# Kernel optimization log

Measured on AMD Instinct MI355X. Metric: run time of the kernel, lower is better.

## Reference

```python
import jax, jax.numpy as jnp
import numpy as np

N = 100_000      # nodes
E = 1_600_000    # edges (no self loops; reference appends them)
G = 1_000        # graphs
FIN = 27         # input node features
HID = 128        # hidden_channels
L = 4            # num_layers
H = 8            # num_heads
B = 4            # num_bases
A = 3            # aggregators: sum, mean, max
FH = HID // H    # per-head out dim
EPS = 1e-5


def setup_inputs() -> dict:
    key = jax.random.key(0)
    ks = jax.random.split(key, 16)
    s = 0.05
    x = jax.random.normal(ks[0], (N, FIN), jnp.float32)
    src = jax.random.randint(ks[1], (E,), 0, N)
    off = jax.random.randint(ks[2], (E,), 1, N)
    dst = (src + off) % N  # guaranteed no self loops
    edge_index = jnp.stack([src, dst]).astype(jnp.int64)
    batch = jnp.sort(jax.random.randint(ks[3], (N,), 0, G)).astype(jnp.int64)
    return {
        "x": x,
        "lin1_w": jax.random.normal(ks[4], (FIN, HID), jnp.float32) * s,
        "lin1_b": jnp.zeros((HID,), jnp.float32),
        "bn1_g": jnp.ones((HID,), jnp.float32),
        "bn1_b": jnp.zeros((HID,), jnp.float32),
        "bases_w": jax.random.normal(ks[5], (L, HID, B * FH), jnp.float32) * s,
        "comb_w": jax.random.normal(ks[6], (L, HID, H * B * A), jnp.float32) * s,
        "comb_b": jnp.zeros((L, H * B * A), jnp.float32),
        "conv_bias": jnp.zeros((L, HID), jnp.float32),
        "bn_g": jnp.ones((L, HID), jnp.float32),
        "bn_b": jnp.zeros((L, HID), jnp.float32),
        "mlp_w1": jax.random.normal(ks[7], (HID, HID // 2), jnp.float32) * s,
        "mbn1_g": jnp.ones((HID // 2,), jnp.float32),
        "mbn1_b": jnp.zeros((HID // 2,), jnp.float32),
        "mlp_w2": jax.random.normal(ks[8], (HID // 2, HID // 4), jnp.float32) * s,
        "mbn2_g": jnp.ones((HID // 4,), jnp.float32),
        "mbn2_b": jnp.zeros((HID // 4,), jnp.float32),
        "mlp_w3": jax.random.normal(ks[9], (HID // 4, 10), jnp.float32) * s,
        "mlp_b3": jnp.zeros((10,), jnp.float32),
        "edge_index": edge_index,
        "batch": batch,
    }


def _bn(h, g, b):
    # BatchNorm1d, training mode (biased batch variance), per-feature over nodes
    mu = jnp.mean(h, axis=0)
    var = jnp.mean((h - mu) ** 2, axis=0)
    return g * (h - mu) * jax.lax.rsqrt(var + EPS) + b


def reference(x, lin1_w, lin1_b, bn1_g, bn1_b, bases_w, comb_w, comb_b,
              conv_bias, bn_g, bn_b, mlp_w1, mbn1_g, mbn1_b, mlp_w2,
              mbn2_g, mbn2_b, mlp_w3, mlp_b3, edge_index, batch):
    # add self loops (inputs contain none, matching remove+add in EGConv)
    loop = jnp.arange(N, dtype=edge_index.dtype)
    src = jnp.concatenate([edge_index[0], loop])
    dst = jnp.concatenate([edge_index[1], loop])

    h = jax.nn.relu(_bn(x @ lin1_w + lin1_b, bn1_g, bn1_b))  # [N, HID]

    ones_e = jnp.ones((src.shape[0], 1), h.dtype)
    deg = jax.ops.segment_sum(ones_e, dst, num_segments=N)  # [N,1], >=1 via self loops

    for l in range(L):
        bases = h @ bases_w[l]                              # [N, B*FH]
        comb = (h @ comb_w[l] + comb_b[l]).reshape(N, H, A * B)
        msg = bases[src]                                    # [E+N, B*FH]
        ssum = jax.ops.segment_sum(msg, dst, num_segments=N)
        smean = ssum / deg
        smax = jax.ops.segment_max(msg, dst, num_segments=N)
        agg = jnp.stack([ssum, smean, smax], axis=1)        # [N, A, B*FH]
        agg = agg.reshape(N, A * B, FH)
        out = jnp.einsum('nhk,nkf->nhf', comb, agg).reshape(N, HID) + conv_bias[l]
        h = h + jax.nn.relu(_bn(out, bn_g[l], bn_b[l]))

    # global mean pool over graphs
    gsum = jax.ops.segment_sum(h, batch, num_segments=G)
    gcnt = jnp.maximum(jax.ops.segment_sum(jnp.ones((N, 1), h.dtype), batch, num_segments=G), 1.0)
    g = gsum / gcnt                                         # [G, HID]

    g = jax.nn.relu(_bn(g @ mlp_w1, mbn1_g, mbn1_b))
    g = jax.nn.relu(_bn(g @ mlp_w2, mbn2_g, mbn2_b))
    return g @ mlp_w3 + mlp_b3                              # [G, 10]
```

## Files before the change

### kernel.cpp

```cpp
#include <hip/hip_runtime.h>

#define EPSV 1e-5f
#define NEGINF -3.402823466e38f
#define NBMAX 1600
#define CHUNK 8192
#define CAP3 6144

typedef short bf16x8 __attribute__((ext_vector_type(8)));
typedef float f32x4 __attribute__((ext_vector_type(4)));

__device__ __forceinline__ unsigned short f2bf(float f) {
    union { float f; unsigned i; } c; c.f = f;
    unsigned r = c.i + 0x7fff + ((c.i >> 16) & 1);
    return (unsigned short)(r >> 16);
}
__device__ __forceinline__ float blo(unsigned u) {
    union { unsigned i; float f; } c; c.i = u << 16; return c.f;
}
__device__ __forceinline__ float bhi(unsigned u) {
    union { unsigned i; float f; } c; c.i = u & 0xffff0000u; return c.f;
}

__global__ __launch_bounds__(256)
void k_lin1(const float* __restrict__ x, const float* __restrict__ w,
            const float* __restrict__ bvec, float* __restrict__ outb,
            float* __restrict__ stats, int N)
{
    __shared__ float wl[27 * 128];
    int tid = threadIdx.x;
    for (int i = tid; i < 27 * 128; i += 256) wl[i] = w[i];
    __syncthreads();

    int l  = tid & 63;
    int wv = tid >> 6;
    float bv0 = bvec[l], bv1 = bvec[64 + l];
    int waveSlots = gridDim.x * 4;
    int trips = (N + waveSlots - 1) / waveSlots;
    float s0 = 0.f, q0 = 0.f, s1 = 0.f, q1 = 0.f;
    for (int it = 0; it < trips; ++it) {
        int n = (it * gridDim.x + blockIdx.x) * 4 + wv;
        if (n < N) {
            const float* xr = x + (size_t)n * 27;
            float a0 = bv0, a1 = bv1;
            #pragma unroll
            for (int k = 0; k < 27; ++k) {
                float xv = xr[k];
                a0 = fmaf(xv, wl[k * 128 + l], a0);
                a1 = fmaf(xv, wl[k * 128 + 64 + l], a1);
            }
            outb[(size_t)n * 128 + l] = a0;
            outb[(size_t)n * 128 + 64 + l] = a1;
            s0 += a0; q0 += a0 * a0; s1 += a1; q1 += a1 * a1;
        }
    }
    __shared__ float sred[4][256];
    sred[0][tid] = s0; sred[1][tid] = q0;
    sred[2][tid] = s1; sred[3][tid] = q1;
    __syncthreads();
    if (tid < 64) {
        int t = tid;
        float v0 = sred[0][t] + sred[0][t + 64] + sred[0][t + 128] + sred[0][t + 192];
        float v1 = sred[1][t] + sred[1][t + 64] + sred[1][t + 128] + sred[1][t + 192];
        float v2 = sred[2][t] + sred[2][t + 64] + sred[2][t + 128] + sred[2][t + 192];
        float v3 = sred[3][t] + sred[3][t + 64] + sred[3][t + 128] + sred[3][t + 192];
        atomicAdd(stats + t, v0);
        atomicAdd(stats + 128 + t, v1);
        atomicAdd(stats + 64 + t, v2);
        atomicAdd(stats + 192 + t, v3);
    }
}

__global__ __launch_bounds__(256)
void k_p1_hist(const int* __restrict__ dst, int* __restrict__ bcnt,
               int E, int NB, int shift)
{
    __shared__ int hist[NBMAX];
    for (int i = threadIdx.x; i < NB; i += 256) hist[i] = 0;
    __syncthreads();
    int stride = gridDim.x * 256;
    for (int e = blockIdx.x * 256 + threadIdx.x; e < E; e += stride)
        atomicAdd(&hist[dst[e] >> shift], 1);
    __syncthreads();
    for (int i = threadIdx.x; i < NB; i += 256)
        if (hist[i]) atomicAdd(bcnt + i, hist[i]);
}

__global__ void k_scan1(const int* __restrict__ cnt, int* __restrict__ rowptr,
                        int* __restrict__ bsum, int N)
{
    __shared__ int sb[256];
    int i = blockIdx.x * 256 + threadIdx.x;
    int v = (i < N) ? cnt[i] : 0;
    sb[threadIdx.x] = v;
    __syncthreads();
    for (int ofs = 1; ofs < 256; ofs <<= 1) {
        int u = (threadIdx.x >= ofs) ? sb[threadIdx.x - ofs] : 0;
        __syncthreads();
        sb[threadIdx.x] += u;
        __syncthreads();
    }
    if (i < N) rowptr[i] = sb[threadIdx.x] - v;
    if (threadIdx.x == 255) bsum[blockIdx.x] = sb[255];
}

__global__ void k_scan2(int* __restrict__ bs, int nb)
{
    __shared__ int sb[512];
    int t = threadIdx.x;
    int v = (t < nb) ? bs[t] : 0;
    sb[t] = v;
    __syncthreads();
    for (int ofs = 1; ofs < 512; ofs <<= 1) {
        int u = (t >= ofs) ? sb[t - ofs] : 0;
        __syncthreads();
        sb[t] += u;
        __syncthreads();
    }
    bs[t] = sb[t] - v;
}

__global__ void k_scan3(int* __restrict__ rowptr, const int* __restrict__ bsum,
                        int N, int E)
{
    int i = blockIdx.x * blockDim.x + threadIdx.x;
    if (i < N) rowptr[i] += bsum[i >> 8];
    if (i == 0) rowptr[N] = E;
}

__global__ __launch_bounds__(256)
void k_p2_scatter(const int* __restrict__ src, const int* __restrict__ dst,
                  const int* __restrict__ bbase, int* __restrict__ bcur0,
                  uint2* __restrict__ bucketed, int E, int NB, int shift)
{
    __shared__ uint2 ebuf[CHUNK];
    __shared__ int hist[NBMAX];
    __shared__ int cur[NBMAX];
    __shared__ int wtmp[256];
    int tid = threadIdx.x;
    int c0 = blockIdx.x * CHUNK;
    int cc = min(CHUNK, E - c0);
    if (cc <= 0) return;

    for (int i = tid; i < NB; i += 256) hist[i] = 0;
    __syncthreads();
    for (int i = tid; i < cc; i += 256)
        atomicAdd(&hist[dst[c0 + i] >> shift], 1);
    __syncthreads();
    int per = (NB + 255) / 256;
    int beg = tid * per, end = min(beg + per, NB);
    int s = 0;
    for (int i = beg; i < end; ++i) s += hist[i];
    wtmp[tid] = s;
    __syncthreads();
    for (int ofs = 1; ofs < 256; ofs <<= 1) {
        int u = (tid >= ofs) ? wtmp[tid - ofs] : 0;
        __syncthreads();
        wtmp[tid] += u;
        __syncthreads();
    }
    int run = wtmp[tid] - s;
    for (int i = beg; i < end; ++i) { cur[i] = run; run += hist[i]; }
    __syncthreads();
    for (int i = tid; i < cc; i += 256) {
        int sv = src[c0 + i], dv = dst[c0 + i];
        int b = dv >> shift;
        int pos = atomicAdd(&cur[b], 1);
        ebuf[pos] = make_uint2((unsigned)sv, (unsigned)dv);
    }
    __syncthreads();
    for (int b = tid; b < NB; b += 256) {
        int c = hist[b];
        if (c > 0) {
            int lb = cur[b] - c;
            int gb = bbase[b] + atomicAdd(&bcur0[b], c);
            hist[b] = gb - lb;
        }
    }
    __syncthreads();
    for (int i = tid; i < cc; i += 256) {
        uint2 u = ebuf[i];
        int b = (int)(u.y >> shift);
        bucketed[hist[b] + i] = u;
    }
}

__global__ __launch_bounds__(256)
void k_p3_csr(const uint2* __restrict__ bucketed, const int* __restrict__ bbase,
              int* __restrict__ rowptr, int* __restrict__ csr,
              int N, int NB, int shift)
{
    __shared__ int ncnt[128], nsc[128];
    __shared__ int lcsr[CAP3];
    int b = blockIdx.x;
    int tid = threadIdx.x;
    int e0 = bbase[b], e1 = bbase[b + 1];
    int cnt = e1 - e0;
    int node0 = b << shift;
    int nodes = min(1 << shift, N - node0);

    if (tid < 128) ncnt[tid] = 0;
    __syncthreads();
    for (int i = tid; i < cnt; i += 256)
        atomicAdd(&ncnt[(int)bucketed[e0 + i].y - node0], 1);
    __syncthreads();
    if (tid < 128) nsc[tid] = ncnt[tid];
    __syncthreads();
    for (int ofs = 1; ofs < 128; ofs <<= 1) {
        int u = 0;
        if (tid < 128 && tid >= ofs) u = nsc[tid - ofs];
        __syncthreads();
        if (tid < 128) nsc[tid] += u;
        __syncthreads();
    }
    if (tid < nodes) rowptr[node0 + tid] = e0 + nsc[tid] - ncnt[tid];
    if (tid == 0 && b == NB - 1) rowptr[N] = e1;
    if (tid < 128) ncnt[tid] = nsc[tid] - ncnt[tid];
    __syncthreads();
    if (cnt <= CAP3) {
        for (int i = tid; i < cnt; i += 256) {
            uint2 u = bucketed[e0 + i];
            int d = (int)u.y - node0;
            int pos = atomicAdd(&ncnt[d], 1);
            lcsr[pos] = (int)u.x;
        }
        __syncthreads();
        for (int i = tid; i < cnt; i += 256) csr[e0 + i] = lcsr[i];
    } else {
        for (int i = tid; i < cnt; i += 256) {
            uint2 u = bucketed[e0 + i];
            int d = (int)u.y - node0;
            int pos = atomicAdd(&ncnt[d], 1);
            csr[e0 + pos] = (int)u.x;
        }
    }
}

__global__ __launch_bounds__(256)
void k_gemm_mfma(const float* __restrict__ tin, float* __restrict__ h,
                 const float* __restrict__ stats, const float* __restrict__ gamma,
                 const float* __restrict__ beta, float invN, int residual,
                 const float* __restrict__ basesW, const float* __restrict__ combW,
                 const float* __restrict__ combB,
                 unsigned short* __restrict__ basesP,
                 unsigned short* __restrict__ combB16, int N)
{
    __shared__ unsigned short Wlds[2560 * 8];
    __shared__ float scL[128], shL[128];
    int tid = threadIdx.x;
    if (tid < 128) {
        float mu  = stats[tid] * invN;
        float var = stats[128 + tid] * invN - mu * mu;
        float sc  = gamma[tid] * rsqrtf(var + EPSV);
        scL[tid] = sc;
        shL[tid] = beta[tid] - mu * sc;
    }
    for (int i = tid; i < 2560; i += 256) {
        int ct = i >> 8, rem = i & 255;
        int ln = rem & 63;
        int n16 = ln & 15, quad = ln >> 4;
        int k = ((rem >> 6) << 5) + quad * 8;
        unsigned short tmp[8];
        if (ct < 4) {
            int c = ct * 16 + n16;
            #pragma unroll
            for (int j = 0; j < 8; ++j) tmp[j] = f2bf(basesW[(k + j) * 64 + c]);
        } else {
            int c = (ct - 4) * 16 + n16;
            #pragma unroll
            for (int j = 0; j < 8; ++j) tmp[j] = f2bf(combW[(k + j) * 96 + c]);
        }
        uint4 pk;
        pk.x = (unsigned)tmp[0] | ((unsigned)tmp[1] << 16);
        pk.y = (unsigned)tmp[2] | ((unsigned)tmp[3] << 16);
        pk.z = (unsigned)tmp[4] | ((unsigned)tmp[5] << 16);
        pk.w = (unsigned)tmp[6] | ((unsigned)tmp[7] << 16);
        *(uint4*)&Wlds[(size_t)i * 8] = pk;
    }
    __syncthreads();

    int lane = tid & 63, wv = tid >> 6;
    int f = lane & 15, quad = lane >> 4;
    float cbv[6];
    #pragma unroll
    for (int s = 0; s < 6; ++s) cbv[s] = combB[s * 16 + f];

    int tiles = (N + 15) >> 4;
    int waveSlots = gridDim.x * 4;
    for (int tile = blockIdx.x * 4 + wv; tile < tiles; tile += waveSlots) {
        int tb = tile * 16;
        int mnode = min(tb + f, N - 1);
        size_t rbase = (size_t)mnode * 128;

        f32x4 acc[10];
        #pragma unroll
        for (int ct = 0; ct < 10; ++ct) acc[ct] = (f32x4){0.f, 0.f, 0.f, 0.f};

        #pragma unroll
        for (int ki = 0; ki < 4; ++ki) {
            int kc = quad * 8 + ki * 32;
            float4 t0 = *(const float4*)&tin[rbase + kc];
            float4 t1 = *(const float4*)&tin[rbase + kc + 4];
            float4 r0, r1;
            r0.x = fmaxf(t0.x * scL[kc]     + shL[kc],     0.f);
            r0.y = fmaxf(t0.y * scL[kc + 1] + shL[kc + 1], 0.f);
            r0.z = fmaxf(t0.z * scL[kc + 2] + shL[kc + 2], 0.f);
            r0.w = fmaxf(t0.w * scL[kc + 3] + shL[kc + 3], 0.f);
            r1.x = fmaxf(t1.x * scL[kc + 4] + shL[kc + 4], 0.f);
            r1.y = fmaxf(t1.y * scL[kc + 5] + shL[kc + 5], 0.f);
            r1.z = fmaxf(t1.z * scL[kc + 6] + shL[kc + 6], 0.f);
            r1.w = fmaxf(t1.w * scL[kc + 7] + shL[kc + 7], 0.f);
            if (residual) {
                float4 h0 = *(const float4*)&h[rbase + kc];
                float4 h1 = *(const float4*)&h[rbase + kc + 4];
                r0.x += h0.x; r0.y += h0.y; r0.z += h0.z; r0.w += h0.w;
                r1.x += h1.x; r1.y += h1.y; r1.z += h1.z; r1.w += h1.w;
            }
            *(float4*)&h[rbase + kc] = r0;
            *(float4*)&h[rbase + kc + 4] = r1;
            short ab[8];
            ab[0] = (short)f2bf(r0.x); ab[1] = (short)f2bf(r0.y);
            ab[2] = (short)f2bf(r0.z); ab[3] = (short)f2bf(r0.w);
            ab[4] = (short)f2bf(r1.x); ab[5] = (short)f2bf(r1.y);
            ab[6] = (short)f2bf(r1.z); ab[7] = (short)f2bf(r1.w);
            bf16x8 a = *(bf16x8*)ab;
            #pragma unroll
            for (int ct = 0; ct < 10; ++ct) {
                bf16x8 bfr = *(const bf16x8*)&Wlds[(size_t)((ct * 4 + ki) * 64 + lane) * 8];
                acc[ct] = __builtin_amdgcn_mfma_f32_16x16x32_bf16(a, bfr, acc[ct], 0, 0, 0);
            }
        }

        #pragma unroll
        for (int r = 0; r < 4; ++r) {
            int node = tb + quad * 4 + r;
            if (node < N) {
                #pragma unroll
                for (int ct = 0; ct < 4; ++ct)
                    basesP[(size_t)node * 64 + f * 4 + ct] = f2bf(acc[ct][r]);
                #pragma unroll
                for (int s = 0; s < 6; ++s)
                    combB16[(size_t)node * 96 + s * 16 + f] = f2bf(acc[4 + s][r] + cbv[s]);
            }
        }
    }
}

__global__ __launch_bounds__(256)
void k_agg(const unsigned short* __restrict__ basesP, const unsigned short* __restrict__ combB16,
           const int* __restrict__ csr, const int* __restrict__ rowptr,
           const float* __restrict__ cbias, float* __restrict__ outb,
           float* __restrict__ stats, int N)
{
    int l = threadIdx.x & 63;
    int w = threadIdx.x >> 6;
    int f = l & 15, sub = l >> 4;
    const char* bp = (const char*)basesP;
    unsigned fof = (unsigned)(f << 3);
    float cb0 = cbias[l], cb1 = cbias[64 + l];
    int waveSlots = gridDim.x * 4;
    int trips = (N + waveSlots - 1) / waveSlots;
    float s0 = 0.f, q0 = 0.f, s1 = 0.f, q1 = 0.f;

    for (int it = 0; it < trips; ++it) {
        int n = (it * gridDim.x + blockIdx.x) * 4 + w;
        if (n < N) {
            int row0 = rowptr[n], row1 = rowptr[n + 1];
            int cnt = row1 - row0;
            float S0 = 0.f, S1 = 0.f, S2 = 0.f, S3 = 0.f;
            float M0 = NEGINF, M1 = NEGINF, M2 = NEGINF, M3 = NEGINF;
            const int* cs = csr + row0 + sub;
            int tfull = cnt >> 2;
            #pragma unroll 4
            for (int t = 0; t < tfull; ++t) {
                int sn = cs[4 * t];
                uint2 u = *(const uint2*)(bp + (((unsigned)sn) << 7) + fof);
                float v0 = blo(u.x), v1 = bhi(u.x), v2 = blo(u.y), v3 = bhi(u.y);
                S0 += v0; S1 += v1; S2 += v2; S3 += v3;
                M0 = fmaxf(M0, v0); M1 = fmaxf(M1, v1);
                M2 = fmaxf(M2, v2); M3 = fmaxf(M3, v3);
            }
            int rem = cnt & 3;
            if (rem) {
                int e = (cnt & ~3) + sub;
                int sn = csr[row0 + min(e, cnt - 1)];
                uint2 u = *(const uint2*)(bp + (((unsigned)sn) << 7) + fof);
                if (sub < rem) {
                    float v0 = blo(u.x), v1 = bhi(u.x), v2 = blo(u.y), v3 = bhi(u.y);
                    S0 += v0; S1 += v1; S2 += v2; S3 += v3;
                    M0 = fmaxf(M0, v0); M1 = fmaxf(M1, v1);
                    M2 = fmaxf(M2, v2); M3 = fmaxf(M3, v3);
                }
            }
            S0 += __shfl_xor(S0, 16, 64); S1 += __shfl_xor(S1, 16, 64);
            S2 += __shfl_xor(S2, 16, 64); S3 += __shfl_xor(S3, 16, 64);
            S0 += __shfl_xor(S0, 32, 64); S1 += __shfl_xor(S1, 32, 64);
            S2 += __shfl_xor(S2, 32, 64); S3 += __shfl_xor(S3, 32, 64);
            M0 = fmaxf(M0, __shfl_xor(M0, 16, 64)); M1 = fmaxf(M1, __shfl_xor(M1, 16, 64));
            M2 = fmaxf(M2, __shfl_xor(M2, 16, 64)); M3 = fmaxf(M3, __shfl_xor(M3, 16, 64));
            M0 = fmaxf(M0, __shfl_xor(M0, 32, 64)); M1 = fmaxf(M1, __shfl_xor(M1, 32, 64));
            M2 = fmaxf(M2, __shfl_xor(M2, 32, 64)); M3 = fmaxf(M3, __shfl_xor(M3, 32, 64));
            uint2 su = *(const uint2*)(bp + (((unsigned)n) << 7) + fof);
            float w0 = blo(su.x), w1 = bhi(su.x), w2 = blo(su.y), w3 = bhi(su.y);
            S0 += w0; S1 += w1; S2 += w2; S3 += w3;
            M0 = fmaxf(M0, w0); M1 = fmaxf(M1, w1);
            M2 = fmaxf(M2, w2); M3 = fmaxf(M3, w3);
            float invd = 1.f / (float)(cnt + 1);
            float A0 = S0 * invd, A1 = S1 * invd, A2 = S2 * invd, A3 = S3 * invd;

            const unsigned short* cr = combB16 + (size_t)n * 96;
            const uint2* c0p = (const uint2*)(cr + sub * 12);
            const uint2* c1p = (const uint2*)(cr + 48 + sub * 12);
            uint2 qa0 = c0p[0], qa1 = c0p[1], qa2 = c0p[2];
            uint2 qb0 = c1p[0], qb1 = c1p[1], qb2 = c1p[2];

            float o0 = cb0, o1 = cb1;
            o0 = fmaf(blo(qa0.x), S0, o0); o0 = fmaf(bhi(qa0.x), S1, o0);
            o0 = fmaf(blo(qa0.y), S2, o0); o0 = fmaf(bhi(qa0.y), S3, o0);
            o0 = fmaf(blo(qa1.x), A0, o0); o0 = fmaf(bhi(qa1.x), A1, o0);
            o0 = fmaf(blo(qa1.y), A2, o0); o0 = fmaf(bhi(qa1.y), A3, o0);
            o0 = fmaf(blo(qa2.x), M0, o0); o0 = fmaf(bhi(qa2.x), M1, o0);
            o0 = fmaf(blo(qa2.y), M2, o0); o0 = fmaf(bhi(qa2.y), M3, o0);
            o1 = fmaf(blo(qb0.x), S0, o1); o1 = fmaf(bhi(qb0.x), S1, o1);
            o1 = fmaf(blo(qb0.y), S2, o1); o1 = fmaf(bhi(qb0.y), S3, o1);
            o1 = fmaf(blo(qb1.x), A0, o1); o1 = fmaf(bhi(qb1.x), A1, o1);
            o1 = fmaf(blo(qb1.y), A2, o1); o1 = fmaf(bhi(qb1.y), A3, o1);
            o1 = fmaf(blo(qb2.x), M0, o1); o1 = fmaf(bhi(qb2.x), M1, o1);
            o1 = fmaf(blo(qb2.y), M2, o1); o1 = fmaf(bhi(qb2.y), M3, o1);

            outb[(size_t)n * 128 + l] = o0;
            outb[(size_t)n * 128 + 64 + l] = o1;
            s0 += o0; q0 += o0 * o0; s1 += o1; q1 += o1 * o1;
        }
    }
    __shared__ float sred[4][256];
    sred[0][threadIdx.x] = s0; sred[1][threadIdx.x] = q0;
    sred[2][threadIdx.x] = s1; sred[3][threadIdx.x] = q1;
    __syncthreads();
    if (threadIdx.x < 64) {
        int t = threadIdx.x;
        float v0 = sred[0][t] + sred[0][t + 64] + sred[0][t + 128] + sred[0][t + 192];
        float v1 = sred[1][t] + sred[1][t + 64] + sred[1][t + 128] + sred[1][t + 192];
        float v2 = sred[2][t] + sred[2][t + 64] + sred[2][t + 128] + sred[2][t + 192];
        float v3 = sred[3][t] + sred[3][t + 64] + sred[3][t + 128] + sred[3][t + 192];
        atomicAdd(stats + t, v0);
        atomicAdd(stats + 128 + t, v1);
        atomicAdd(stats + 64 + t, v2);
        atomicAdd(stats + 192 + t, v3);
    }
}

__global__ void k_gbound(const int* __restrict__ batch, int* __restrict__ gstart,
                         int N, int G)
{
    int stride = gridDim.x * blockDim.x;
    for (int n = blockIdx.x * blockDim.x + threadIdx.x; n < N; n += stride) {
        int b = batch[n];
        if (n == 0) {
            for (int g = 0; g <= b; ++g) gstart[g] = 0;
        } else {
            int pb = batch[n - 1];
            for (int g = pb + 1; g <= b; ++g) gstart[g] = n;
        }
        if (n == N - 1) {
            for (int g = b + 1; g <= G; ++g) gstart[g] = N;
        }
    }
}

__global__ __launch_bounds__(256)
void k_gmean(const float* __restrict__ t, const float* __restrict__ h,
             const float* __restrict__ stats, const float* __restrict__ gamma,
             const float* __restrict__ beta, float invN,
             const int* __restrict__ gstart, float* __restrict__ gout, int G)
{
    __shared__ float part[128];
    int g = blockIdx.x;
    if (g >= G) return;
    int c = threadIdx.x & 127;
    int half = threadIdx.x >> 7;
    float mu  = stats[c] * invN;
    float var = stats[128 + c] * invN - mu * mu;
    float sc  = gamma[c] * rsqrtf(var + EPSV);
    float sh  = beta[c] - mu * sc;
    int s = gstart[g], e = gstart[g + 1];
    float acc = 0.f;
    #pragma unroll 2
    for (int n = s + half; n < e; n += 2) {
        size_t o = (size_t)n * 128 + c;
        acc += h[o] + fmaxf(t[o] * sc + sh, 0.f);
    }
    if (half) part[c] = acc;
    __syncthreads();
    if (!half) {
        float tot = acc + part[c];
        float cntf = fmaxf((float)(e - s), 1.f);
        gout[g * 128 + c] = tot / cntf;
    }
}

__global__ void k_mlp1(const float* __restrict__ gin, const float* __restrict__ w1,
                       float* __restrict__ t1, float* __restrict__ stats, int G)
{
    int g = blockIdx.x;
    int c = threadIdx.x;
    const float* gr = gin + g * 128;
    float acc = 0.f;
    for (int k = 0; k < 128; ++k) acc = fmaf(gr[k], w1[k * 64 + c], acc);
    t1[g * 64 + c] = acc;
    atomicAdd(stats + c, acc);
    atomicAdd(stats + 64 + c, acc * acc);
}

__global__ void k_mlp2(const float* __restrict__ t1, const float* __restrict__ stats1,
                       const float* __restrict__ g1, const float* __restrict__ b1,
                       const float* __restrict__ w2, float* __restrict__ t2,
                       float* __restrict__ stats2, float invG, int G)
{
    __shared__ float row[64];
    int g = blockIdx.x;
    int c = threadIdx.x;
    float v = t1[g * 64 + c];
    float mu = stats1[c] * invG;
    float var = stats1[64 + c] * invG - mu * mu;
    row[c] = fmaxf(g1[c] * (v - mu) * rsqrtf(var + EPSV) + b1[c], 0.f);
    __syncthreads();
    if (c < 32) {
        float acc = 0.f;
        #pragma unroll
        for (int k = 0; k < 64; ++k) acc = fmaf(row[k], w2[k * 32 + c], acc);
        t2[g * 32 + c] = acc;
        atomicAdd(stats2 + c, acc);
        atomicAdd(stats2 + 32 + c, acc * acc);
    }
}

__global__ void k_mlp3(const float* __restrict__ t2, const float* __restrict__ stats2,
                       const float* __restrict__ g2, const float* __restrict__ b2,
                       const float* __restrict__ w3, const float* __restrict__ b3,
                       float* __restrict__ out, float invG, int G)
{
    __shared__ float row[32];
    int g = blockIdx.x;
    int c = threadIdx.x;
    if (c < 32) {
        float v = t2[g * 32 + c];
        float mu = stats2[c] * invG;
        float var = stats2[32 + c] * invG - mu * mu;
        row[c] = fmaxf(g2[c] * (v - mu) * rsqrtf(var + EPSV) + b2[c], 0.f);
    }
    __syncthreads();
    if (c < 10) {
        float acc = b3[c];
        #pragma unroll
        for (int k = 0; k < 32; ++k) acc = fmaf(row[k], w3[k * 10 + c], acc);
        out[g * 10 + c] = acc;
    }
}

extern "C" void kernel_launch(void* const* d_in, const int* in_sizes, int n_in,
                              void* d_out, int out_size, void* d_ws, size_t ws_size,
                              hipStream_t stream)
{
    const float* x        = (const float*)d_in[0];
    const float* lin1_w   = (const float*)d_in[1];
    const float* lin1_b   = (const float*)d_in[2];
    const float* bn1_g    = (const float*)d_in[3];
    const float* bn1_b    = (const float*)d_in[4];
    const float* bases_w  = (const float*)d_in[5];
    const float* comb_w   = (const float*)d_in[6];
    const float* comb_b   = (const float*)d_in[7];
    const float* conv_bias= (const float*)d_in[8];
    const float* bn_g     = (const float*)d_in[9];
    const float* bn_b     = (const float*)d_in[10];
    const float* mlp_w1   = (const float*)d_in[11];
    const float* mbn1_g   = (const float*)d_in[12];
    const float* mbn1_b   = (const float*)d_in[13];
    const float* mlp_w2   = (const float*)d_in[14];
    const float* mbn2_g   = (const float*)d_in[15];
    const float* mbn2_b   = (const float*)d_in[16];
    const float* mlp_w3   = (const float*)d_in[17];
    const float* mlp_b3   = (const float*)d_in[18];
    const int*   edge_idx = (const int*)d_in[19];
    const int*   batch    = (const int*)d_in[20];
    float* outp = (float*)d_out;

    const int N = in_sizes[20];
    const int E = in_sizes[19] / 2;
    const int G = out_size / 10;
    const int* esrc = edge_idx;
    const int* edst = edge_idx + E;

    int shift = 6;
    while ((((N - 1) >> shift) + 1) > NBMAX && shift < 7) ++shift;
    const int NB = ((N - 1) >> shift) + 1;

    char* p = (char*)d_ws;
    auto alloc = [&](size_t bytes) {
        char* r = p;
        p += (bytes + 255) & ~(size_t)255;
        return r;
    };
    float*          h      = (float*)alloc((size_t)N * 128 * 4);
    unsigned short* basesP = (unsigned short*)alloc((size_t)N * 64 * 2);
    unsigned short* combB16= (unsigned short*)alloc((size_t)N * 96 * 2);
    float*          outb   = (float*)alloc((size_t)N * 128 * 4);
    int*            csr    = (int*)  alloc((size_t)E * 4);
    int*            rowptr = (int*)  alloc((size_t)(N + 1) * 4);
    int*            bbase  = (int*)  alloc((size_t)(NB + 1) * 4);
    float*          tg     = (float*)alloc((size_t)G * 128 * 4);
    float*          t1     = (float*)alloc((size_t)G * 64 * 4);
    float*          t2     = (float*)alloc((size_t)G * 32 * 4);
    int*            gstart = (int*)  alloc((size_t)(G + 1) * 4);
    int*            bsum   = (int*)  alloc(512 * 4);
    char*           zbase  = p;
    int*            bcnt   = (int*)  alloc((size_t)NB * 4);
    int*            bcur0  = (int*)  alloc((size_t)NB * 4);
    float*          stats  = (float*)alloc(7 * 256 * 4);
    size_t zbytes = (size_t)(p - zbase);
    uint2* bucketed = (uint2*)combB16;
    (void)ws_size; (void)n_in;

    hipMemsetAsync(zbase, 0, zbytes, stream);

    const float invN = 1.0f / (float)N;
    const float invG = 1.0f / (float)G;
    const int nbB = (NB + 255) / 256;

    k_lin1<<<1024, 256, 0, stream>>>(x, lin1_w, lin1_b, outb, stats, N);
    k_p1_hist<<<256, 256, 0, stream>>>(edst, bcnt, E, NB, shift);
    k_scan1<<<nbB, 256, 0, stream>>>(bcnt, bbase, bsum, NB);
    k_scan2<<<1, 512, 0, stream>>>(bsum, nbB);
    k_scan3<<<nbB, 256, 0, stream>>>(bbase, bsum, NB, E);
    k_p2_scatter<<<(E + CHUNK - 1) / CHUNK, 256, 0, stream>>>(esrc, edst, bbase, bcur0,
                                                              bucketed, E, NB, shift);
    k_p3_csr<<<NB, 256, 0, stream>>>(bucketed, bbase, rowptr, csr, N, NB, shift);

    for (int l = 0; l < 4; ++l) {
        const float* bw = bases_w + (size_t)l * 128 * 64;
        const float* cw = comb_w + (size_t)l * 128 * 96;
        const float* cb = comb_b + (size_t)l * 96;
        const float* cvb = conv_bias + (size_t)l * 128;
        const float* pg = (l == 0) ? bn1_g : bn_g + (l - 1) * 128;
        const float* pb = (l == 0) ? bn1_b : bn_b + (l - 1) * 128;
        k_gemm_mfma<<<512, 256, 0, stream>>>(outb, h, stats + l * 256, pg, pb, invN,
                                             l > 0 ? 1 : 0, bw, cw, cb, basesP, combB16, N);
        k_agg<<<2048, 256, 0, stream>>>(basesP, combB16, csr, rowptr, cvb,
                                        outb, stats + (1 + l) * 256, N);
    }

    k_gbound<<<512, 256, 0, stream>>>(batch, gstart, N, G);
    k_gmean<<<G, 256, 0, stream>>>(outb, h, stats + 4 * 256, bn_g + 3 * 128,
                                   bn_b + 3 * 128, invN, gstart, tg, G);
    float* st5 = stats + 5 * 256;
    float* st6 = stats + 6 * 256;
    k_mlp1<<<G, 64, 0, stream>>>(tg, mlp_w1, t1, st5, G);
    k_mlp2<<<G, 64, 0, stream>>>(t1, st5, mbn1_g, mbn1_b, mlp_w2, t2, st6, invG, G);
    k_mlp3<<<G, 64, 0, stream>>>(t2, st6, mbn2_g, mbn2_b, mlp_w3, mlp_b3, outp, invG, G);
}
```

Before: 818.1 us.

## Store pre-BN conv output in bf16 and batch four nodes per wave in aggregation

The intermediate pre-BatchNorm buffer (outb) is now stored as bf16 instead of fp32, which halves its write and read traffic in lin1, agg, gemm and gmean. The aggregation kernel now gives each wave four consecutive nodes and interleaves their neighbor gathers, so more independent loads are in flight per wave. It launches one block per 16 nodes instead of using a grid-stride loop. In exchange, the BN input loses precision, and nodes with uneven degrees waste lanes because each wave loops to the largest count among its four nodes.

```diff
diff --git a/kernel.cpp b/kernel.cpp
--- a/kernel.cpp
+++ b/kernel.cpp
@@ -20,10 +20,13 @@
 __device__ __forceinline__ float bhi(unsigned u) {
     union { unsigned i; float f; } c; c.i = u & 0xffff0000u; return c.f;
 }
+__device__ __forceinline__ float bfu(unsigned short u) {
+    union { unsigned i; float f; } c; c.i = ((unsigned)u) << 16; return c.f;
+}
 
 __global__ __launch_bounds__(256)
 void k_lin1(const float* __restrict__ x, const float* __restrict__ w,
-            const float* __restrict__ bvec, float* __restrict__ outb,
+            const float* __restrict__ bvec, unsigned short* __restrict__ outb,
             float* __restrict__ stats, int N)
 {
     __shared__ float wl[27 * 128];
@@ -48,8 +51,8 @@
                 a0 = fmaf(xv, wl[k * 128 + l], a0);
                 a1 = fmaf(xv, wl[k * 128 + 64 + l], a1);
             }
-            outb[(size_t)n * 128 + l] = a0;
-            outb[(size_t)n * 128 + 64 + l] = a1;
+            outb[(size_t)n * 128 + l] = f2bf(a0);
+            outb[(size_t)n * 128 + 64 + l] = f2bf(a1);
             s0 += a0; q0 += a0 * a0; s1 += a1; q1 += a1 * a1;
         }
     }
@@ -236,7 +239,7 @@
 }
 
 __global__ __launch_bounds__(256)
-void k_gemm_mfma(const float* __restrict__ tin, float* __restrict__ h,
+void k_gemm_mfma(const unsigned short* __restrict__ tin, float* __restrict__ h,
                  const float* __restrict__ stats, const float* __restrict__ gamma,
                  const float* __restrict__ beta, float invN, int residual,
                  const float* __restrict__ basesW, const float* __restrict__ combW,
@@ -298,30 +301,29 @@
         #pragma unroll
         for (int ki = 0; ki < 4; ++ki) {
             int kc = quad * 8 + ki * 32;
-            float4 t0 = *(const float4*)&tin[rbase + kc];
-            float4 t1 = *(const float4*)&tin[rbase + kc + 4];
-            float4 r0, r1;
-            r0.x = fmaxf(t0.x * scL[kc]     + shL[kc],     0.f);
-            r0.y = fmaxf(t0.y * scL[kc + 1] + shL[kc + 1], 0.f);
-            r0.z = fmaxf(t0.z * scL[kc + 2] + shL[kc + 2], 0.f);
-            r0.w = fmaxf(t0.w * scL[kc + 3] + shL[kc + 3], 0.f);
-            r1.x = fmaxf(t1.x * scL[kc + 4] + shL[kc + 4], 0.f);
-            r1.y = fmaxf(t1.y * scL[kc + 5] + shL[kc + 5], 0.f);
-            r1.z = fmaxf(t1.z * scL[kc + 6] + shL[kc + 6], 0.f);
-            r1.w = fmaxf(t1.w * scL[kc + 7] + shL[kc + 7], 0.f);
+            uint4 tv = *(const uint4*)&tin[rbase + kc];
+            float r0, r1, r2, r3, r4, r5, r6, r7;
+            r0 = fmaxf(blo(tv.x) * scL[kc]     + shL[kc],     0.f);
+            r1 = fmaxf(bhi(tv.x) * scL[kc + 1] + shL[kc + 1], 0.f);
+            r2 = fmaxf(blo(tv.y) * scL[kc + 2] + shL[kc + 2], 0.f);
+            r3 = fmaxf(bhi(tv.y) * scL[kc + 3] + shL[kc + 3], 0.f);
+            r4 = fmaxf(blo(tv.z) * scL[kc + 4] + shL[kc + 4], 0.f);
+            r5 = fmaxf(bhi(tv.z) * scL[kc + 5] + shL[kc + 5], 0.f);
+            r6 = fmaxf(blo(tv.w) * scL[kc + 6] + shL[kc + 6], 0.f);
+            r7 = fmaxf(bhi(tv.w) * scL[kc + 7] + shL[kc + 7], 0.f);
             if (residual) {
                 float4 h0 = *(const float4*)&h[rbase + kc];
                 float4 h1 = *(const float4*)&h[rbase + kc + 4];
-                r0.x += h0.x; r0.y += h0.y; r0.z += h0.z; r0.w += h0.w;
-                r1.x += h1.x; r1.y += h1.y; r1.z += h1.z; r1.w += h1.w;
+                r0 += h0.x; r1 += h0.y; r2 += h0.z; r3 += h0.w;
+                r4 += h1.x; r5 += h1.y; r6 += h1.z; r7 += h1.w;
             }
-            *(float4*)&h[rbase + kc] = r0;
-            *(float4*)&h[rbase + kc + 4] = r1;
+            *(float4*)&h[rbase + kc]     = make_float4(r0, r1, r2, r3);
+            *(float4*)&h[rbase + kc + 4] = make_float4(r4, r5, r6, r7);
             short ab[8];
-            ab[0] = (short)f2bf(r0.x); ab[1] = (short)f2bf(r0.y);
-            ab[2] = (short)f2bf(r0.z); ab[3] = (short)f2bf(r0.w);
-            ab[4] = (short)f2bf(r1.x); ab[5] = (short)f2bf(r1.y);
-            ab[6] = (short)f2bf(r1.z); ab[7] = (short)f2bf(r1.w);
+            ab[0] = (short)f2bf(r0); ab[1] = (short)f2bf(r1);
+            ab[2] = (short)f2bf(r2); ab[3] = (short)f2bf(r3);
+            ab[4] = (short)f2bf(r4); ab[5] = (short)f2bf(r5);
+            ab[6] = (short)f2bf(r6); ab[7] = (short)f2bf(r7);
             bf16x8 a = *(bf16x8*)ab;
             #pragma unroll
             for (int ct = 0; ct < 10; ++ct) {
@@ -348,7 +350,7 @@
 __global__ __launch_bounds__(256)
 void k_agg(const unsigned short* __restrict__ basesP, const unsigned short* __restrict__ combB16,
            const int* __restrict__ csr, const int* __restrict__ rowptr,
-           const float* __restrict__ cbias, float* __restrict__ outb,
+           const float* __restrict__ cbias, unsigned short* __restrict__ outb,
            float* __restrict__ stats, int N)
 {
     int l = threadIdx.x & 63;
@@ -356,80 +358,103 @@
     int f = l & 15, sub = l >> 4;
     const char* bp = (const char*)basesP;
     unsigned fof = (unsigned)(f << 3);
-    float cb0 = cbias[l], cb1 = cbias[64 + l];
-    int waveSlots = gridDim.x * 4;
-    int trips = (N + waveSlots - 1) / waveSlots;
     float s0 = 0.f, q0 = 0.f, s1 = 0.f, q1 = 0.f;
 
-    for (int it = 0; it < trips; ++it) {
-        int n = (it * gridDim.x + blockIdx.x) * 4 + w;
-        if (n < N) {
-            int row0 = rowptr[n], row1 = rowptr[n + 1];
-            int cnt = row1 - row0;
-            float S0 = 0.f, S1 = 0.f, S2 = 0.f, S3 = 0.f;
-            float M0 = NEGINF, M1 = NEGINF, M2 = NEGINF, M3 = NEGINF;
-            const int* cs = csr + row0 + sub;
-            int tfull = cnt >> 2;
-            #pragma unroll 4
-            for (int t = 0; t < tfull; ++t) {
-                int sn = cs[4 * t];
-                uint2 u = *(const uint2*)(bp + (((unsigned)sn) << 7) + fof);
-                float v0 = blo(u.x), v1 = bhi(u.x), v2 = blo(u.y), v3 = bhi(u.y);
-                S0 += v0; S1 += v1; S2 += v2; S3 += v3;
-                M0 = fmaxf(M0, v0); M1 = fmaxf(M1, v1);
-                M2 = fmaxf(M2, v2); M3 = fmaxf(M3, v3);
+    int base = (blockIdx.x * 4 + w) * 4;
+    if (base < N) {
+        float cb0 = cbias[l], cb1 = cbias[64 + l];
+        int row0[4], cnt[4];
+        #pragma unroll
+        for (int m = 0; m < 4; ++m) {
+            int nm = min(base + m, N - 1);
+            row0[m] = rowptr[nm];
+            cnt[m]  = rowptr[nm + 1] - row0[m];
+            if (base + m >= N) cnt[m] = 0;
+        }
+        float S[4][4], M[4][4];
+        #pragma unroll
+        for (int m = 0; m < 4; ++m) {
+            #pragma unroll
+            for (int v = 0; v < 4; ++v) { S[m][v] = 0.f; M[m][v] = NEGINF; }
+        }
+        int mc = max(max(cnt[0], cnt[1]), max(cnt[2], cnt[3]));
+        int mt = (mc + 3) >> 2;
+        int e = sub;
+        #pragma unroll 2
+        for (int t = 0; t < mt; ++t) {
+            int sn[4];
+            #pragma unroll
+            for (int m = 0; m < 4; ++m) {
+                int ce = min(e, cnt[m] - 1);
+                ce = max(ce, 0);
+                sn[m] = csr[row0[m] + ce];
             }
-            int rem = cnt & 3;
-            if (rem) {
-                int e = (cnt & ~3) + sub;
-                int sn = csr[row0 + min(e, cnt - 1)];
-                uint2 u = *(const uint2*)(bp + (((unsigned)sn) << 7) + fof);
-                if (sub < rem) {
-                    float v0 = blo(u.x), v1 = bhi(u.x), v2 = blo(u.y), v3 = bhi(u.y);
-                    S0 += v0; S1 += v1; S2 += v2; S3 += v3;
-                    M0 = fmaxf(M0, v0); M1 = fmaxf(M1, v1);
-                    M2 = fmaxf(M2, v2); M3 = fmaxf(M3, v3);
-                }
+            uint2 u[4];
+            #pragma unroll
+            for (int m = 0; m < 4; ++m)
+                u[m] = *(const uint2*)(bp + (((unsigned)sn[m]) << 7) + fof);
+            #pragma unroll
+            for (int m = 0; m < 4; ++m) {
+                bool val = e < cnt[m];
+                float v0 = blo(u[m].x), v1 = bhi(u[m].x);
+                float v2 = blo(u[m].y), v3 = bhi(u[m].y);
+                S[m][0] += val ? v0 : 0.f;
+                S[m][1] += val ? v1 : 0.f;
+                S[m][2] += val ? v2 : 0.f;
+                S[m][3] += val ? v3 : 0.f;
+                M[m][0] = fmaxf(M[m][0], val ? v0 : NEGINF);
+                M[m][1] = fmaxf(M[m][1], val ? v1 : NEGINF);
+                M[m][2] = fmaxf(M[m][2], val ? v2 : NEGINF);
+                M[m][3] = fmaxf(M[m][3], val ? v3 : NEGINF);
             }
-            S0 += __shfl_xor(S0, 16, 64); S1 += __shfl_xor(S1, 16, 64);
-            S2 += __shfl_xor(S2, 16, 64); S3 += __shfl_xor(S3, 16, 64);
-            S0 += __shfl_xor(S0, 32, 64); S1 += __shfl_xor(S1, 32, 64);
-            S2 += __shfl_xor(S2, 32, 64); S3 += __shfl_xor(S3, 32, 64);
-            M0 = fmaxf(M0, __shfl_xor(M0, 16, 64)); M1 = fmaxf(M1, __shfl_xor(M1, 16, 64));
-            M2 = fmaxf(M2, __shfl_xor(M2, 16, 64)); M3 = fmaxf(M3, __shfl_xor(M3, 16, 64));
-            M0 = fmaxf(M0, __shfl_xor(M0, 32, 64)); M1 = fmaxf(M1, __shfl_xor(M1, 32, 64));
-            M2 = fmaxf(M2, __shfl_xor(M2, 32, 64)); M3 = fmaxf(M3, __shfl_xor(M3, 32, 64));
-            uint2 su = *(const uint2*)(bp + (((unsigned)n) << 7) + fof);
-            float w0 = blo(su.x), w1 = bhi(su.x), w2 = blo(su.y), w3 = bhi(su.y);
-            S0 += w0; S1 += w1; S2 += w2; S3 += w3;
-            M0 = fmaxf(M0, w0); M1 = fmaxf(M1, w1);
-            M2 = fmaxf(M2, w2); M3 = fmaxf(M3, w3);
-            float invd = 1.f / (float)(cnt + 1);
-            float A0 = S0 * invd, A1 = S1 * invd, A2 = S2 * invd, A3 = S3 * invd;
-
-            const unsigned short* cr = combB16 + (size_t)n * 96;
-            const uint2* c0p = (const uint2*)(cr + sub * 12);
-            const uint2* c1p = (const uint2*)(cr + 48 + sub * 12);
-            uint2 qa0 = c0p[0], qa1 = c0p[1], qa2 = c0p[2];
-            uint2 qb0 = c1p[0], qb1 = c1p[1], qb2 = c1p[2];
-
-            float o0 = cb0, o1 = cb1;
-            o0 = fmaf(blo(qa0.x), S0, o0); o0 = fmaf(bhi(qa0.x), S1, o0);
-            o0 = fmaf(blo(qa0.y), S2, o0); o0 = fmaf(bhi(qa0.y), S3, o0);
-            o0 = fmaf(blo(qa1.x), A0, o0); o0 = fmaf(bhi(qa1.x), A1, o0);
-            o0 = fmaf(blo(qa1.y), A2, o0); o0 = fmaf(bhi(qa1.y), A3, o0);
-            o0 = fmaf(blo(qa2.x), M0, o0); o0 = fmaf(bhi(qa2.x), M1, o0);
-            o0 = fmaf(blo(qa2.y), M2, o0); o0 = fmaf(bhi(qa2.y), M3, o0);
-            o1 = fmaf(blo(qb0.x), S0, o1); o1 = fmaf(bhi(qb0.x), S1, o1);
-            o1 = fmaf(blo(qb0.y), S2, o1); o1 = fmaf(bhi(qb0.y), S3, o1);
-            o1 = fmaf(blo(qb1.x), A0, o1); o1 = fmaf(bhi(qb1.x), A1, o1);
-            o1 = fmaf(blo(qb1.y), A2, o1); o1 = fmaf(bhi(qb1.y), A3, o1);
-            o1 = fmaf(blo(qb2.x), M0, o1); o1 = fmaf(bhi(qb2.x), M1, o1);
-            o1 = fmaf(blo(qb2.y), M2, o1); o1 = fmaf(bhi(qb2.y), M3, o1);
-
-            outb[(size_t)n * 128 + l] = o0;
-            outb[(size_t)n * 128 + 64 + l] = o1;
-            s0 += o0; q0 += o0 * o0; s1 += o1; q1 += o1 * o1;
+            e += 4;
+        }
+        #pragma unroll
+        for (int m = 0; m < 4; ++m) {
+            int n = base + m;
+            if (n < N) {
+                float T0 = S[m][0], T1 = S[m][1], T2 = S[m][2], T3 = S[m][3];
+                float X0 = M[m][0], X1 = M[m][1], X2 = M[m][2], X3 = M[m][3];
+                T0 += __shfl_xor(T0, 16, 64); T1 += __shfl_xor(T1, 16, 64);
+                T2 += __shfl_xor(T2, 16, 64); T3 += __shfl_xor(T3, 16, 64);
+                T0 += __shfl_xor(T0, 32, 64); T1 += __shfl_xor(T1, 32, 64);
+                T2 += __shfl_xor(T2, 32, 64); T3 += __shfl_xor(T3, 32, 64);
+                X0 = fmaxf(X0, __shfl_xor(X0, 16, 64)); X1 = fmaxf(X1, __shfl_xor(X1, 16, 64));
+                X2 = fmaxf(X2, __shfl_xor(X2, 16, 64)); X3 = fmaxf(X3, __shfl_xor(X3, 16, 64));
+                X0 = fmaxf(X0, __shfl_xor(X0, 32, 64)); X1 = fmaxf(X1, __shfl_xor(X1, 32, 64));
+                X2 = fmaxf(X2, __shfl_xor(X2, 32, 64)); X3 = fmaxf(X3, __shfl_xor(X3, 32, 64));
+                uint2 su = *(const uint2*)(bp + (((unsigned)n) << 7) + fof);
+                float w0 = blo(su.x), w1 = bhi(su.x), w2 = blo(su.y), w3 = bhi(su.y);
+                T0 += w0; T1 += w1; T2 += w2; T3 += w3;
+                X0 = fmaxf(X0, w0); X1 = fmaxf(X1, w1);
+                X2 = fmaxf(X2, w2); X3 = fmaxf(X3, w3);
+                float invd = 1.f / (float)(cnt[m] + 1);
+                float A0 = T0 * invd, A1 = T1 * invd, A2 = T2 * invd, A3 = T3 * invd;
+
+                const unsigned short* cr = combB16 + (size_t)n * 96;
+                const uint2* c0p = (const uint2*)(cr + sub * 12);
+                const uint2* c1p = (const uint2*)(cr + 48 + sub * 12);
+                uint2 qa0 = c0p[0], qa1 = c0p[1], qa2 = c0p[2];
+                uint2 qb0 = c1p[0], qb1 = c1p[1], qb2 = c1p[2];
+
+                float o0 = cb0, o1 = cb1;
+                o0 = fmaf(blo(qa0.x), T0, o0); o0 = fmaf(bhi(qa0.x), T1, o0);
+                o0 = fmaf(blo(qa0.y), T2, o0); o0 = fmaf(bhi(qa0.y), T3, o0);
+                o0 = fmaf(blo(qa1.x), A0, o0); o0 = fmaf(bhi(qa1.x), A1, o0);
+                o0 = fmaf(blo(qa1.y), A2, o0); o0 = fmaf(bhi(qa1.y), A3, o0);
+                o0 = fmaf(blo(qa2.x), X0, o0); o0 = fmaf(bhi(qa2.x), X1, o0);
+                o0 = fmaf(blo(qa2.y), X2, o0); o0 = fmaf(bhi(qa2.y), X3, o0);
+                o1 = fmaf(blo(qb0.x), T0, o1); o1 = fmaf(bhi(qb0.x), T1, o1);
+                o1 = fmaf(blo(qb0.y), T2, o1); o1 = fmaf(bhi(qb0.y), T3, o1);
+                o1 = fmaf(blo(qb1.x), A0, o1); o1 = fmaf(bhi(qb1.x), A1, o1);
+                o1 = fmaf(blo(qb1.y), A2, o1); o1 = fmaf(bhi(qb1.y), A3, o1);
+                o1 = fmaf(blo(qb2.x), X0, o1); o1 = fmaf(bhi(qb2.x), X1, o1);
+                o1 = fmaf(blo(qb2.y), X2, o1); o1 = fmaf(bhi(qb2.y), X3, o1);
+
+                outb[(size_t)n * 128 + l] = f2bf(o0);
+                outb[(size_t)n * 128 + 64 + l] = f2bf(o1);
+                s0 += o0; q0 += o0 * o0; s1 += o1; q1 += o1 * o1;
+            }
         }
     }
     __shared__ float sred[4][256];
@@ -468,7 +493,7 @@
 }
 
 __global__ __launch_bounds__(256)
-void k_gmean(const float* __restrict__ t, const float* __restrict__ h,
+void k_gmean(const unsigned short* __restrict__ t, const float* __restrict__ h,
              const float* __restrict__ stats, const float* __restrict__ gamma,
              const float* __restrict__ beta, float invN,
              const int* __restrict__ gstart, float* __restrict__ gout, int G)
@@ -487,7 +512,7 @@
     #pragma unroll 2
     for (int n = s + half; n < e; n += 2) {
         size_t o = (size_t)n * 128 + c;
-        acc += h[o] + fmaxf(t[o] * sc + sh, 0.f);
+        acc += h[o] + fmaxf(bfu(t[o]) * sc + sh, 0.f);
     }
     if (half) part[c] = acc;
     __syncthreads();
@@ -603,8 +628,8 @@
     float*          h      = (float*)alloc((size_t)N * 128 * 4);
     unsigned short* basesP = (unsigned short*)alloc((size_t)N * 64 * 2);
     unsigned short* combB16= (unsigned short*)alloc((size_t)N * 96 * 2);
-    float*          outb   = (float*)alloc((size_t)N * 128 * 4);
-    int*            csr    = (int*)  alloc((size_t)E * 4);
+    unsigned short* outb   = (unsigned short*)alloc((size_t)N * 128 * 2);
+    int*            csr    = (int*)  alloc((size_t)(E + 64) * 4);
     int*            rowptr = (int*)  alloc((size_t)(N + 1) * 4);
     int*            bbase  = (int*)  alloc((size_t)(NB + 1) * 4);
     float*          tg     = (float*)alloc((size_t)G * 128 * 4);
@@ -635,6 +660,7 @@
                                                               bucketed, E, NB, shift);
     k_p3_csr<<<NB, 256, 0, stream>>>(bucketed, bbase, rowptr, csr, N, NB, shift);
 
+    const int aggBlocks = (N + 15) / 16;
     for (int l = 0; l < 4; ++l) {
         const float* bw = bases_w + (size_t)l * 128 * 64;
         const float* cw = comb_w + (size_t)l * 128 * 96;
@@ -644,8 +670,8 @@
         const float* pb = (l == 0) ? bn1_b : bn_b + (l - 1) * 128;
         k_gemm_mfma<<<512, 256, 0, stream>>>(outb, h, stats + l * 256, pg, pb, invN,
                                              l > 0 ? 1 : 0, bw, cw, cb, basesP, combB16, N);
-        k_agg<<<2048, 256, 0, stream>>>(basesP, combB16, csr, rowptr, cvb,
-                                        outb, stats + (1 + l) * 256, N);
+        k_agg<<<aggBlocks, 256, 0, stream>>>(basesP, combB16, csr, rowptr, cvb,
+                                             outb, stats + (1 + l) * 256, N);
     }
 
     k_gbound<<<512, 256, 0, stream>>>(batch, gstart, N, G);
```

Result: slower. 1.082 ms (+32.2%).
